# Performance work log

Hardware: AMD Instinct MI355X
Metric: run time of the kernel (lower is better)

The kernel has to match this reference:

```python
import jax, jax.numpy as jnp
import numpy as np

B, N, D, H = 8, 1024, 512, 8
DK = D // H  # key_dim == val_dim == 64
LN_EPS = 1e-5


def setup_inputs() -> dict:
    key = jax.random.key(0)
    ks = jax.random.split(key, 16)
    stdv = 1.0 / np.sqrt(D)
    u = lambda k, shape, s: jax.random.uniform(k, shape, jnp.float32, -s, s)
    inp = {
        'q': jax.random.normal(ks[0], (B, N, D), jnp.float32),
        'mask': jax.random.uniform(ks[1], (B, N, N)) < 0.1,  # True = masked out
        # eps1 is torch.zeros in the source (never re-initialized); use small
        'eps1': jax.random.normal(ks[2], (D, D), jnp.float32) * 0.03,
        # 3 MLP layers, stacked on leading axis. Linear: y = x @ W.T + b
        'U_w': u(ks[3], (3, D, D), stdv), 'U_b': u(ks[4], (3, D), stdv),
        'V_w': u(ks[5], (3, D, D), stdv), 'V_b': u(ks[6], (3, D), stdv),
        'ln_g': jnp.ones((3, D), jnp.float32), 'ln_b': jnp.zeros((3, D), jnp.float32),
        'W_query': u(ks[7], (H, D, DK), 1.0 / np.sqrt(DK)),
        'W_key':   u(ks[8], (H, D, DK), 1.0 / np.sqrt(DK)),
        'W_val':   u(ks[9], (H, D, DK), 1.0 / np.sqrt(DK)),
        'W_out':   u(ks[10], (H, DK, D), stdv),
    }
    return inp


def _layer_norm(x, g, b):
    mu = jnp.mean(x, axis=-1, keepdims=True)
    var = jnp.mean(jnp.square(x - mu), axis=-1, keepdims=True)
    return (x - mu) * jax.lax.rsqrt(var + LN_EPS) * g + b


def _mlp_layer(x, Uw, Ub, Vw, Vb, g, b):
    # U1 -> (identity maxpool k=1) -> V1 -> LayerNorm -> ReLU -> residual
    y = x @ Uw.T + Ub
    y = y @ Vw.T + Vb
    y = _layer_norm(y, g, b)
    return x + jax.nn.relu(y)


def reference(q, mask, eps1, U_w, U_b, V_w, V_b, ln_g, ln_b,
              W_query, W_key, W_val, W_out):
    nf = 1.0 / np.sqrt(DK)  # norm_factor; applied to BOTH Q and K as in source
    h = q
    for l in range(3):
        h = _mlp_layer(h @ eps1, U_w[l], U_b[l], V_w[l], V_b[l], ln_g[l], ln_b[l])
    # per-head projections: (H,B,N,DK)
    Q = jnp.einsum('bqd,hdk->hbqk', q, W_query) * nf
    K = jnp.einsum('bgd,hdk->hbgk', h, W_key) * nf
    V = jnp.einsum('bgd,hdk->hbgk', h, W_val)
    scores = jnp.einsum('hbqk,hbgk->hbqg', Q, K)  # (H,B,N,N)
    scores = jnp.where(mask[None], -1e10, scores)
    attn = jax.nn.softmax(scores, axis=-1)
    heads = jnp.einsum('hbqg,hbgv->hbqv', attn, V)
    out = jnp.einsum('hbqv,hvd->bqd', heads, W_out)  # (B,N,D)
    return out
```

## Files before the change

kernel.cpp:

```cpp
#include <hip/hip_runtime.h>

typedef __attribute__((ext_vector_type(8))) short bhalf8;
typedef __attribute__((ext_vector_type(4))) short bhalf4;
typedef __attribute__((ext_vector_type(4))) float f32x4;

__device__ __forceinline__ ushort f2bf(float f) {
  unsigned u = __builtin_bit_cast(unsigned, f);
  unsigned r = u + 0x7fffu + ((u >> 16) & 1u);
  return (ushort)(r >> 16);
}

__device__ __forceinline__ void gld16(const ushort* g, ushort* l) {
  __builtin_amdgcn_global_load_lds((const __attribute__((address_space(1))) void*)g,
                                   (__attribute__((address_space(3))) void*)l, 16, 0, 0);
}

__global__ __launch_bounds__(256) void prep_kernel(
    const float* __restrict__ q, const int* __restrict__ mask,
    const float* __restrict__ eps1, const float* __restrict__ U_w,
    const float* __restrict__ V_w, const float* __restrict__ Wq,
    const float* __restrict__ Wk, const float* __restrict__ Wv,
    const float* __restrict__ Wo, const float* __restrict__ U_b,
    const float* __restrict__ V_b,
    ushort* __restrict__ qb, unsigned long long* __restrict__ minv,
    ushort* __restrict__ uwb, ushort* __restrict__ vwb,
    ushort* __restrict__ e1b, ushort* __restrict__ e1t,
    ushort* __restrict__ wqkv, ushort* __restrict__ wot,
    float* __restrict__ cvec) {
  int i = blockIdx.x * 256 + threadIdx.x;
  if (i < 4194304) {
    qb[i] = f2bf(q[i]);
  } else if (i < 12582912) {
    int j = i - 4194304;
    unsigned long long bb = __ballot(mask[j] != 0);
    if ((threadIdx.x & 63) == 0) {
      int b = j >> 20, qq = (j >> 10) & 1023, g = j & 1023;
      minv[((size_t)b * 16 + (g >> 6)) * 1024 + qq] = ~bb;
    }
  } else if (i < 13369344) {
    int j = i - 12582912;
    uwb[j] = f2bf(U_w[j]);
  } else if (i < 14155776) {
    int j = i - 13369344;
    vwb[j] = f2bf(V_w[j]);
  } else if (i < 14417920) {
    int j = i - 14155776;
    e1b[j] = f2bf(eps1[j]);
  } else if (i < 14680064) {
    int j = i - 14417920; int n = j >> 9, k = j & 511;
    e1t[j] = f2bf(eps1[k * 512 + n]);
  } else if (i < 15466496) {
    int j = i - 14680064; int n = j >> 9, d = j & 511;
    const float* W = (n < 512) ? Wq : (n < 1024 ? Wk : Wv);
    float sc = (n < 512) ? 0.02255252509f : 1.0f;
    int nl = n & 511;
    wqkv[j] = f2bf(W[((nl >> 6) * 512 + d) * 64 + (nl & 63)] * sc);
  } else if (i < 15728640) {
    int j = i - 15466496; int d = j >> 9, hv = j & 511;
    wot[j] = f2bf(Wo[hv * 512 + d]);
  } else {
    int j = i - 15728640;
    int idx = j >> 6, ln = j & 63;
    int l = idx >> 9;
    const float* vr = V_w + (size_t)idx * 512 + ln * 8;
    const float* ur = U_b + l * 512 + ln * 8;
    float s = 0;
#pragma unroll
    for (int t = 0; t < 8; t++) s += vr[t] * ur[t];
#pragma unroll
    for (int off = 1; off < 64; off <<= 1) s += __shfl_xor(s, off, 64);
    if (ln == 0) cvec[idx] = s + V_b[idx];
  }
}

template <int BN>
__global__ __launch_bounds__(256) void gemm_nt(
    const ushort* __restrict__ A0, const ushort* __restrict__ A1,
    const ushort* __restrict__ Bt0, const ushort* __restrict__ Bt1,
    int bsplit, int mstride, int M, int K,
    ushort* __restrict__ Oa, const float* __restrict__ ba, int ca,
    ushort* __restrict__ Ob, const float* __restrict__ bb2, int cb,
    ushort* __restrict__ Oc, const float* __restrict__ bc, int cc) {
  __shared__ ushort As[128 * 32];
  __shared__ ushort Bs[BN * 32];
  int tid = threadIdx.x;
  int wave = tid >> 6, lane = tid & 63;
  int quad = lane >> 4, col = lane & 15;
  int m0 = blockIdx.x * 128, n0 = blockIdx.y * BN;
  const ushort* A = (A1 && n0 >= 512) ? A1 : A0;
  const ushort* Bp = ((n0 < bsplit) ? Bt0 + (size_t)n0 * K
                                    : Bt1 + (size_t)(n0 - bsplit) * K) +
                     (size_t)(m0 >> 9) * mstride;
  constexpr int NI = BN / 32;
  int wm = (BN == 128) ? (wave >> 1) * 64 : (wave & 1) * 64;
  int wn = (BN == 128) ? (wave & 1) * 64 : (wave >> 1) * 32;
  f32x4 acc[4][NI] = {};
  int srow = wave * 16 + (lane >> 2);
  int skc = (lane & 3) * 8;
  const ushort* gA0 = A + (size_t)(m0 + srow) * K + skc;
  const ushort* gA1 = gA0 + (size_t)64 * K;
  const ushort* gB0 = Bp + (size_t)srow * K + skc;
  const ushort* gB1 = gB0 + (size_t)64 * K;
  ushort* lA0 = &As[wave * 16 * 32];
  ushort* lA1 = &As[(64 + wave * 16) * 32];
  ushort* lB0 = &Bs[wave * 16 * 32];
  ushort* lB1 = (BN == 128) ? &Bs[(64 + wave * 16) * 32] : nullptr;

  gld16(gA0, lA0);
  gld16(gA1, lA1);
  gld16(gB0, lB0);
  if (BN == 128) gld16(gB1, lB1);

  for (int k0 = 0; k0 < K; k0 += 32) {
    __syncthreads();
    bhalf8 af[4], bg[NI];
#pragma unroll
    for (int i = 0; i < 4; i++)
      af[i] = *(bhalf8*)&As[(wm + i * 16 + col) * 32 + quad * 8];
#pragma unroll
    for (int i = 0; i < NI; i++)
      bg[i] = *(bhalf8*)&Bs[(wn + i * 16 + col) * 32 + quad * 8];
    __syncthreads();
    if (k0 + 32 < K) {
      gld16(gA0 + k0 + 32, lA0);
      gld16(gA1 + k0 + 32, lA1);
      gld16(gB0 + k0 + 32, lB0);
      if (BN == 128) gld16(gB1 + k0 + 32, lB1);
    }
#pragma unroll
    for (int mi = 0; mi < 4; mi++)
#pragma unroll
      for (int ni = 0; ni < NI; ni++)
        acc[mi][ni] = __builtin_amdgcn_mfma_f32_16x16x32_bf16(af[mi], bg[ni], acc[mi][ni], 0, 0, 0);
  }

  int reg = n0 >> 9;
  ushort* O = (reg == 0) ? Oa : (reg == 1 ? Ob : Oc);
  const float* bs = (reg == 0) ? ba : (reg == 1 ? bb2 : bc);
  int code = (reg == 0) ? ca : (reg == 1 ? cb : cc);
#pragma unroll
  for (int mi = 0; mi < 4; mi++)
#pragma unroll
    for (int ni = 0; ni < NI; ni++) {
      int cn = n0 + wn + ni * 16 + col;
      int cnl = cn & 511;
      int cmb = m0 + wm + mi * 16 + quad * 4;
      float bv = bs ? bs[cnl] : 0.f;
      if (code == 2) {
        int bhh = (cmb >> 10) * 8 + (cnl >> 6);
        size_t base = ((size_t)bhh * 64 + ((cmb & 1023) >> 4)) * 1024 +
                      (size_t)((cnl >> 5) & 1) * 512 + (size_t)(cmb & 15) * 32 + (cnl & 31);
#pragma unroll
        for (int r = 0; r < 4; r++)
          O[base + r * 32] = f2bf(acc[mi][ni][r] + bv);
      } else if (code == 3) {
        int bhh = (cmb >> 10) * 8 + (cnl >> 6);
        size_t base = ((size_t)bhh * 64 + ((cmb & 1023) >> 4)) * 1024 +
                      (size_t)(cnl & 63) * 16 + (cmb & 15);
        ushort4 pk;
        pk.x = f2bf(acc[mi][ni][0] + bv);
        pk.y = f2bf(acc[mi][ni][1] + bv);
        pk.z = f2bf(acc[mi][ni][2] + bv);
        pk.w = f2bf(acc[mi][ni][3] + bv);
        *(ushort4*)&O[base] = pk;
      } else if (code == 1) {
        float* Ff = (float*)O;
#pragma unroll
        for (int r = 0; r < 4; r++)
          Ff[(size_t)(cmb + r) * 512 + cnl] = acc[mi][ni][r] + bv;
      } else {
#pragma unroll
        for (int r = 0; r < 4; r++)
          O[(size_t)(cmb + r) * 512 + cnl] = f2bf(acc[mi][ni][r] + bv);
      }
    }
}

__global__ __launch_bounds__(256) void ln_kernel(
    const float* __restrict__ z, const ushort* __restrict__ tb,
    const float* __restrict__ lgam, const float* __restrict__ lbet,
    ushort* __restrict__ hb) {
  int row = blockIdx.x * 4 + (threadIdx.x >> 6);
  int lane = threadIdx.x & 63;
  int cbase = lane * 8;
  const float* zr = z + (size_t)row * 512 + cbase;
  float x[8];
  *(float4*)&x[0] = *(const float4*)zr;
  *(float4*)&x[4] = *(const float4*)(zr + 4);
  float sum = 0;
#pragma unroll
  for (int i = 0; i < 8; i++) sum += x[i];
#pragma unroll
  for (int off = 1; off < 64; off <<= 1) sum += __shfl_xor(sum, off, 64);
  float mu = sum * (1.f / 512.f);
  float vs = 0;
#pragma unroll
  for (int i = 0; i < 8; i++) { float d = x[i] - mu; vs += d * d; }
#pragma unroll
  for (int off = 1; off < 64; off <<= 1) vs += __shfl_xor(vs, off, 64);
  float rstd = rsqrtf(vs * (1.f / 512.f) + 1e-5f);
  uint4 tr = *(const uint4*)&tb[(size_t)row * 512 + cbase];
  float tv[8];
  {
    const unsigned* u = (const unsigned*)&tr;
#pragma unroll
    for (int w = 0; w < 4; w++) {
      tv[2 * w] = __builtin_bit_cast(float, u[w] << 16);
      tv[2 * w + 1] = __builtin_bit_cast(float, u[w] & 0xFFFF0000u);
    }
  }
  ushort outv[8];
#pragma unroll
  for (int i = 0; i < 8; i++) {
    float val = (x[i] - mu) * rstd * lgam[cbase + i] + lbet[cbase + i];
    outv[i] = f2bf(tv[i] + fmaxf(val, 0.f));
  }
  *(uint4*)&hb[(size_t)row * 512 + cbase] = *(uint4*)outv;
}

__global__ __launch_bounds__(256, 3) void attn_kernel(
    const ushort* __restrict__ QtT, const ushort* __restrict__ KtT,
    const ushort* __restrict__ VtT, const unsigned long long* __restrict__ minv,
    ushort* __restrict__ Op) {
  int bh = blockIdx.x, qt0 = blockIdx.y;
  int b = bh >> 3, h = bh & 7;
  __shared__ float R[64 * 68];
  int tid = threadIdx.x, w = tid >> 6, lane = tid & 63;
  int quad = lane >> 4, col = lane & 15;
  int q0 = qt0 * 64;
  const ushort* Kt = KtT + (size_t)bh * 65536 + col * 32 + quad * 8;
  const ushort* Vt = VtT + (size_t)bh * 65536 + col * 16 + quad * 4;
  const ushort* Qt = QtT + (size_t)bh * 65536 + col * 32 + quad * 8;
  bhalf8 bq[4][2];
#pragma unroll
  for (int qt = 0; qt < 4; qt++)
#pragma unroll
    for (int ks = 0; ks < 2; ks++)
      bq[qt][ks] = *(const bhalf8*)(Qt + (size_t)(qt0 * 4 + qt) * 1024 + ks * 512);
  f32x4 o[4][4] = {};
  float lsum[4] = {0.f, 0.f, 0.f, 0.f};
  const unsigned long long* mb = minv + (size_t)b * 16384 + q0 + col;

  for (int g0 = 0; g0 < 1024; g0 += 128) {
    int gs = g0 + w * 32;
    int gw = gs >> 6;
    int sb = (gs & 32) + quad * 4;
    unsigned shq[4];
#pragma unroll
    for (int qt = 0; qt < 4; qt++)
      shq[qt] = (unsigned)(mb[gw * 1024 + qt * 16] >> sb);
#pragma unroll
    for (int gt = 0; gt < 2; gt++) {
      size_t gblk = (size_t)((gs >> 4) + gt) * 1024;
      bhalf8 ak0 = *(const bhalf8*)(Kt + gblk);
      bhalf8 ak1 = *(const bhalf8*)(Kt + gblk + 512);
      bhalf4 av[4];
#pragma unroll
      for (int vt = 0; vt < 4; vt++)
        av[vt] = *(const bhalf4*)(Vt + gblk + vt * 256);
#pragma unroll
      for (int qt = 0; qt < 4; qt++) {
        f32x4 s = {};
        s = __builtin_amdgcn_mfma_f32_16x16x32_bf16(ak0, bq[qt][0], s, 0, 0, 0);
        s = __builtin_amdgcn_mfma_f32_16x16x32_bf16(ak1, bq[qt][1], s, 0, 0, 0);
        unsigned sh = shq[qt];
        unsigned pu[4];
#pragma unroll
        for (int r = 0; r < 4; r++) {
          const int pos = gt * 16 + r;
          unsigned keep = (unsigned)((int)(sh << (31 - pos)) >> 31);
          pu[r] = __builtin_bit_cast(unsigned, __builtin_amdgcn_exp2f(s[r])) & keep;
          lsum[qt] += __builtin_bit_cast(float, pu[r]);
        }
        uint2 pp;
        pp.x = ((pu[0] + 0x8000u) >> 16) | (((pu[1] + 0x8000u) >> 16) << 16);
        pp.y = ((pu[2] + 0x8000u) >> 16) | (((pu[3] + 0x8000u) >> 16) << 16);
        bhalf4 bp = __builtin_bit_cast(bhalf4, pp);
#pragma unroll
        for (int vt = 0; vt < 4; vt++)
          o[vt][qt] = __builtin_amdgcn_mfma_f32_16x16x16bf16_1k(av[vt], bp, o[vt][qt], 0, 0, 0);
      }
    }
  }
  for (int src = 1; src < 4; src++) {
    __syncthreads();
    if (w == src) {
      float* dst = R + lane * 68;
#pragma unroll
      for (int vt = 0; vt < 4; vt++)
#pragma unroll
        for (int qt = 0; qt < 4; qt++)
          *(f32x4*)(dst + (vt * 4 + qt) * 4) = o[vt][qt];
#pragma unroll
      for (int qt = 0; qt < 4; qt++) dst[64 + qt] = lsum[qt];
    }
    __syncthreads();
    if (w == 0) {
      const float* sp = R + lane * 68;
#pragma unroll
      for (int vt = 0; vt < 4; vt++)
#pragma unroll
        for (int qt = 0; qt < 4; qt++)
          o[vt][qt] += *(const f32x4*)(sp + (vt * 4 + qt) * 4);
#pragma unroll
      for (int qt = 0; qt < 4; qt++) lsum[qt] += sp[64 + qt];
    }
  }
  if (w == 0) {
    float rl[4];
#pragma unroll
    for (int qt = 0; qt < 4; qt++) {
      lsum[qt] += __shfl_xor(lsum[qt], 16, 64);
      lsum[qt] += __shfl_xor(lsum[qt], 32, 64);
      rl[qt] = __builtin_amdgcn_rcpf(lsum[qt]);
    }
#pragma unroll
    for (int vt = 0; vt < 4; vt++)
#pragma unroll
      for (int qt = 0; qt < 4; qt++) {
        ushort4 pk;
        pk.x = f2bf(o[vt][qt][0] * rl[qt]);
        pk.y = f2bf(o[vt][qt][1] * rl[qt]);
        pk.z = f2bf(o[vt][qt][2] * rl[qt]);
        pk.w = f2bf(o[vt][qt][3] * rl[qt]);
        *(ushort4*)&Op[(size_t)(b * 1024 + q0 + qt * 16 + col) * 512 +
                       h * 64 + vt * 16 + quad * 4] = pk;
      }
  }
}

extern "C" void kernel_launch(void* const* d_in, const int* in_sizes, int n_in,
                              void* d_out, int out_size, void* d_ws, size_t ws_size,
                              hipStream_t stream) {
  const float* q    = (const float*)d_in[0];
  const int*   mask = (const int*)d_in[1];
  const float* eps1 = (const float*)d_in[2];
  const float* U_w  = (const float*)d_in[3];
  const float* U_b  = (const float*)d_in[4];
  const float* V_w  = (const float*)d_in[5];
  const float* V_b  = (const float*)d_in[6];
  const float* ln_g = (const float*)d_in[7];
  const float* ln_b = (const float*)d_in[8];
  const float* Wq   = (const float*)d_in[9];
  const float* Wk   = (const float*)d_in[10];
  const float* Wv   = (const float*)d_in[11];
  const float* Wo   = (const float*)d_in[12];
  float* out = (float*)d_out;

  char* ws = (char*)d_ws;
  auto carve = [&](size_t bytes) { char* p = ws; ws += bytes; return p; };
  ushort* qb   = (ushort*)carve(8388608);
  ushort* uwb  = (ushort*)carve(1572864);
  ushort* vwb  = (ushort*)carve(1572864);
  ushort* e1b  = (ushort*)carve(524288);
  ushort* e1t  = (ushort*)carve(524288);
  ushort* wqkv = (ushort*)carve(1572864);
  ushort* wot  = (ushort*)carve(524288);
  ushort* A1b  = (ushort*)carve(1572864);
  ushort* Gtb  = (ushort*)carve(1572864);
  float*  cvec = (float*)carve(6144);
  unsigned long long* minv = (unsigned long long*)carve(1048576);
  ushort* tb   = (ushort*)carve(8388608);
  float*  zf   = (float*)carve(16777216);
  ushort* hb   = (ushort*)carve(8388608);
  ushort* Qtt  = (ushort*)carve(8388608);
  ushort* Ktt  = (ushort*)carve(8388608);
  ushort* Vtt  = (ushort*)carve(8388608);
  ushort* Ob   = (ushort*)carve(8388608);
  const int BIG = 1 << 30;

  prep_kernel<<<61824, 256, 0, stream>>>(q, mask, eps1, U_w, V_w, Wq, Wk, Wv, Wo,
                                         U_b, V_b, qb, minv, uwb, vwb, e1b, e1t,
                                         wqkv, wot, cvec);
  gemm_nt<128><<<dim3(4, 12), 256, 0, stream>>>(
      e1b, nullptr, uwb, nullptr, BIG, 0, 512, 512,
      A1b, nullptr, 0, A1b + 262144, nullptr, 0, A1b + 524288, nullptr, 0);
  gemm_nt<64><<<dim3(12, 8), 256, 0, stream>>>(
      vwb, nullptr, A1b, nullptr, BIG, 262144, 1536, 512,
      Gtb, nullptr, 0, nullptr, nullptr, 0, nullptr, nullptr, 0);
  const ushort* hsrc = qb;
  for (int l = 0; l < 3; l++) {
    gemm_nt<128><<<dim3(64, 8), 256, 0, stream>>>(
        hsrc, nullptr, e1t, Gtb + l * 262144, 512, 0, 8192, 512,
        tb, nullptr, 0, (ushort*)zf, cvec + l * 512, 1, nullptr, nullptr, 0);
    ln_kernel<<<2048, 256, 0, stream>>>(zf, tb, ln_g + l * 512, ln_b + l * 512, hb);
    hsrc = hb;
  }
  gemm_nt<128><<<dim3(64, 12), 256, 0, stream>>>(
      qb, hb, wqkv, nullptr, BIG, 0, 8192, 512,
      Qtt, nullptr, 2, Ktt, nullptr, 2, Vtt, nullptr, 3);
  attn_kernel<<<dim3(64, 16), 256, 0, stream>>>(Qtt, Ktt, Vtt, minv, Ob);
  gemm_nt<64><<<dim3(64, 8), 256, 0, stream>>>(
      Ob, nullptr, wot, nullptr, BIG, 0, 8192, 512,
      (ushort*)out, nullptr, 1, nullptr, nullptr, 0, nullptr, nullptr, 0);
}
```

Before: 308.4 us.

## Double-buffer K/V/mask loads in attention and shrink GEMM tiles for more blocks

The attention kernel now prefetches the next iteration's K, V and mask words into a second register buffer while the current tile's MFMAs run, so global load latency overlaps with compute. It also packs the bf16 probabilities with a byte-permute instruction, and drops the 3-waves-per-SIMD occupancy bound to leave room for the extra registers. Separately, the MLP and QKV GEMMs switch from 128 to 64 tiles with twice as many blocks to fill more CUs. The costs are higher register pressure and lower occupancy in attention, plus less operand reuse per block in the GEMMs.

```diff
diff --git a/kernel.cpp b/kernel.cpp
--- a/kernel.cpp
+++ b/kernel.cpp
@@ -218,7 +218,7 @@
   *(uint4*)&hb[(size_t)row * 512 + cbase] = *(uint4*)outv;
 }
 
-__global__ __launch_bounds__(256, 3) void attn_kernel(
+__global__ __launch_bounds__(256) void attn_kernel(
     const ushort* __restrict__ QtT, const ushort* __restrict__ KtT,
     const ushort* __restrict__ VtT, const unsigned long long* __restrict__ minv,
     ushort* __restrict__ Op) {
@@ -240,45 +240,68 @@
   f32x4 o[4][4] = {};
   float lsum[4] = {0.f, 0.f, 0.f, 0.f};
   const unsigned long long* mb = minv + (size_t)b * 16384 + q0 + col;
-
-  for (int g0 = 0; g0 < 1024; g0 += 128) {
-    int gs = g0 + w * 32;
-    int gw = gs >> 6;
-    int sb = (gs & 32) + quad * 4;
-    unsigned shq[4];
-#pragma unroll
-    for (int qt = 0; qt < 4; qt++)
-      shq[qt] = (unsigned)(mb[gw * 1024 + qt * 16] >> sb);
+  const int sb = (w & 1) * 32 + quad * 4;
+  const int gwoff = (w >> 1);
+
+  bhalf8 kf[2][2][2];
+  bhalf4 vf[2][2][4];
+  unsigned long long mwq[2][4];
+  {
+    int gs = w * 32;
+#pragma unroll
+    for (int qt = 0; qt < 4; qt++) mwq[0][qt] = mb[gwoff * 1024 + qt * 16];
 #pragma unroll
     for (int gt = 0; gt < 2; gt++) {
       size_t gblk = (size_t)((gs >> 4) + gt) * 1024;
-      bhalf8 ak0 = *(const bhalf8*)(Kt + gblk);
-      bhalf8 ak1 = *(const bhalf8*)(Kt + gblk + 512);
-      bhalf4 av[4];
+      kf[0][gt][0] = *(const bhalf8*)(Kt + gblk);
+      kf[0][gt][1] = *(const bhalf8*)(Kt + gblk + 512);
 #pragma unroll
       for (int vt = 0; vt < 4; vt++)
-        av[vt] = *(const bhalf4*)(Vt + gblk + vt * 256);
+        vf[0][gt][vt] = *(const bhalf4*)(Vt + gblk + vt * 256);
+    }
+  }
+#pragma unroll
+  for (int it = 0; it < 8; it++) {
+    const int par = it & 1;
+    if (it < 7) {
+      int gsn = (it + 1) * 128 + w * 32;
+      int gwn = ((it + 1) * 2) + gwoff;
+#pragma unroll
+      for (int qt = 0; qt < 4; qt++) mwq[par ^ 1][qt] = mb[gwn * 1024 + qt * 16];
+#pragma unroll
+      for (int gt = 0; gt < 2; gt++) {
+        size_t gblk = (size_t)((gsn >> 4) + gt) * 1024;
+        kf[par ^ 1][gt][0] = *(const bhalf8*)(Kt + gblk);
+        kf[par ^ 1][gt][1] = *(const bhalf8*)(Kt + gblk + 512);
+#pragma unroll
+        for (int vt = 0; vt < 4; vt++)
+          vf[par ^ 1][gt][vt] = *(const bhalf4*)(Vt + gblk + vt * 256);
+      }
+    }
+#pragma unroll
+    for (int gt = 0; gt < 2; gt++) {
 #pragma unroll
       for (int qt = 0; qt < 4; qt++) {
         f32x4 s = {};
-        s = __builtin_amdgcn_mfma_f32_16x16x32_bf16(ak0, bq[qt][0], s, 0, 0, 0);
-        s = __builtin_amdgcn_mfma_f32_16x16x32_bf16(ak1, bq[qt][1], s, 0, 0, 0);
-        unsigned sh = shq[qt];
-        unsigned pu[4];
+        s = __builtin_amdgcn_mfma_f32_16x16x32_bf16(kf[par][gt][0], bq[qt][0], s, 0, 0, 0);
+        s = __builtin_amdgcn_mfma_f32_16x16x32_bf16(kf[par][gt][1], bq[qt][1], s, 0, 0, 0);
+        unsigned sh = (unsigned)(mwq[par][qt] >> sb);
+        unsigned pr[4];
 #pragma unroll
         for (int r = 0; r < 4; r++) {
           const int pos = gt * 16 + r;
           unsigned keep = (unsigned)((int)(sh << (31 - pos)) >> 31);
-          pu[r] = __builtin_bit_cast(unsigned, __builtin_amdgcn_exp2f(s[r])) & keep;
-          lsum[qt] += __builtin_bit_cast(float, pu[r]);
+          unsigned pu = __builtin_bit_cast(unsigned, __builtin_amdgcn_exp2f(s[r])) & keep;
+          lsum[qt] += __builtin_bit_cast(float, pu);
+          pr[r] = pu + 0x8000u;
         }
         uint2 pp;
-        pp.x = ((pu[0] + 0x8000u) >> 16) | (((pu[1] + 0x8000u) >> 16) << 16);
-        pp.y = ((pu[2] + 0x8000u) >> 16) | (((pu[3] + 0x8000u) >> 16) << 16);
+        pp.x = __builtin_amdgcn_perm(pr[1], pr[0], 0x07060302u);
+        pp.y = __builtin_amdgcn_perm(pr[3], pr[2], 0x07060302u);
         bhalf4 bp = __builtin_bit_cast(bhalf4, pp);
 #pragma unroll
         for (int vt = 0; vt < 4; vt++)
-          o[vt][qt] = __builtin_amdgcn_mfma_f32_16x16x16bf16_1k(av[vt], bp, o[vt][qt], 0, 0, 0);
+          o[vt][qt] = __builtin_amdgcn_mfma_f32_16x16x16bf16_1k(vf[par][gt][vt], bp, o[vt][qt], 0, 0, 0);
       }
     }
   }
@@ -380,13 +403,13 @@
       Gtb, nullptr, 0, nullptr, nullptr, 0, nullptr, nullptr, 0);
   const ushort* hsrc = qb;
   for (int l = 0; l < 3; l++) {
-    gemm_nt<128><<<dim3(64, 8), 256, 0, stream>>>(
+    gemm_nt<64><<<dim3(64, 16), 256, 0, stream>>>(
         hsrc, nullptr, e1t, Gtb + l * 262144, 512, 0, 8192, 512,
         tb, nullptr, 0, (ushort*)zf, cvec + l * 512, 1, nullptr, nullptr, 0);
     ln_kernel<<<2048, 256, 0, stream>>>(zf, tb, ln_g + l * 512, ln_b + l * 512, hb);
     hsrc = hb;
   }
-  gemm_nt<128><<<dim3(64, 12), 256, 0, stream>>>(
+  gemm_nt<64><<<dim3(64, 24), 256, 0, stream>>>(
       qb, hb, wqkv, nullptr, BIG, 0, 8192, 512,
       Qtt, nullptr, 2, Ktt, nullptr, 2, Vtt, nullptr, 3);
   attn_kernel<<<dim3(64, 16), 256, 0, stream>>>(Qtt, Ktt, Vtt, minv, Ob);
```

Measured after the change: 319.9 us. 1.04x slower.
